# Kernel optimization log

Measured on AMD Instinct MI355X. Metric: run time of the kernel, lower is better.

Reference implementation:

```python
import jax, jax.numpy as jnp
import numpy as np

N, E, D, C, L, G = 50000, 1600000, 128, 10, 4, 512
BN_EPS = 1e-5


def setup_inputs() -> dict:
    key = jax.random.key(0)
    ks = jax.random.split(key, 16)
    s = 0.05  # weight init scale
    inp = {
        "x": jax.random.normal(ks[0], (N, D), dtype=jnp.float32),
        "edge_index": jax.random.randint(ks[1], (2, E), 0, N, dtype=jnp.int32),
        "batch": jnp.sort(jax.random.randint(ks[2], (N,), 0, G, dtype=jnp.int32)),
        "num_graphs": G,
        # GINConv inner MLP params (layer 0 input dim == D since num_features == num_hidden)
        "conv_W1": jax.random.normal(ks[3], (L, D, D), dtype=jnp.float32) * s,
        "conv_b1": jnp.zeros((L, D), dtype=jnp.float32),
        "conv_bn_g": jnp.ones((L, D), dtype=jnp.float32),
        "conv_bn_b": jnp.zeros((L, D), dtype=jnp.float32),
        "conv_W2": jax.random.normal(ks[4], (L, D, D), dtype=jnp.float32) * s,
        "conv_b2": jnp.zeros((L, D), dtype=jnp.float32),
        # outer BatchNorm after each conv
        "bn_g": jnp.ones((L, D), dtype=jnp.float32),
        "bn_b": jnp.zeros((L, D), dtype=jnp.float32),
        # per-scale classifier heads (L+1 of them; fcs[0] input dim == num_features == D)
        "fc_W": jax.random.normal(ks[5], (L + 1, D, C), dtype=jnp.float32) * s,
        "fc_b": jnp.zeros((L + 1, C), dtype=jnp.float32),
    }
    return inp


def _bn(h, g, b):
    # BatchNorm1d in training mode: batch stats over nodes, biased variance
    m = h.mean(axis=0)
    v = jnp.mean((h - m) ** 2, axis=0)
    return (h - m) * jax.lax.rsqrt(v + BN_EPS) * g + b


def reference(x, edge_index, batch, num_graphs, conv_W1, conv_b1, conv_bn_g,
              conv_bn_b, conv_W2, conv_b2, bn_g, bn_b, fc_W, fc_b):
    n_nodes = x.shape[0]
    src, dst = edge_index[0], edge_index[1]
    outs = [x]
    h = x
    for i in range(L):
        # GINConv (eps=0, aggr='add'): mlp(x + scatter_add of neighbor features)
        agg = jax.ops.segment_sum(h[src], dst, num_segments=n_nodes)  # [N, D]
        z = h + agg
        z = z @ conv_W1[i] + conv_b1[i]
        z = jax.nn.relu(_bn(z, conv_bn_g[i], conv_bn_b[i]))
        z = z @ conv_W2[i] + conv_b2[i]
        h = jax.nn.relu(_bn(z, bn_g[i], bn_b[i]))
        outs.append(h)
    out = None
    for i, o in enumerate(outs):
        pooled = jax.ops.segment_sum(o, batch, num_segments=num_graphs)  # [G, D]
        logits = pooled @ fc_W[i] + fc_b[i]
        out = logits if out is None else out + logits
    return jax.nn.log_softmax(out, axis=-1)
```

## Files before the change

kernel.cpp:

```cpp
#include <hip/hip_runtime.h>

#define NN 50000
#define EE 1600000
#define DD 128
#define CC 10
#define LLAY 4
#define GG 512
#define GD (GG*DD)
#define NB 196
#define BK_EDGES 1024
#define BUCKCAP 16000
#define NSUB 16
#define SUBW 3125
#define WPAD 136

static constexpr float BN_EPS = 1e-5f;
static constexpr float INV_N = 1.0f / (float)NN;

typedef __bf16 bf16x8 __attribute__((ext_vector_type(8)));
typedef float f32x4 __attribute__((ext_vector_type(4)));

static __device__ __forceinline__ float bflo(unsigned u){ return __uint_as_float(u << 16); }
static __device__ __forceinline__ float bfhi(unsigned u){ return __uint_as_float(u & 0xffff0000u); }
static __device__ __forceinline__ unsigned short f2bf(float f){
    unsigned u = __float_as_uint(f);
    return (unsigned short)((u + 0x7fffu + ((u >> 16) & 1u)) >> 16);
}
static __device__ __forceinline__ unsigned packbf(float a, float b){
    return (unsigned)f2bf(a) | ((unsigned)f2bf(b) << 16);
}
static __device__ __forceinline__ unsigned encf(float f){
    unsigned b = __float_as_uint(f);
    return (b & 0x80000000u) ? ~b : (b | 0x80000000u);
}
static __device__ __forceinline__ float decf(unsigned e){
    unsigned b = (e & 0x80000000u) ? (e ^ 0x80000000u) : ~e;
    return __uint_as_float(b);
}
static __device__ __forceinline__ bf16x8 ldfrag(const unsigned short* p){
    union { uint4 u; bf16x8 b; } t; t.u = *(const uint4*)p; return t.b;
}
static __device__ __forceinline__ bf16x8 asfrag(uint4 u){
    union { uint4 u; bf16x8 b; } t; t.u = u; return t.b;
}


__global__ void zero_k(int* p, int n){
    int i = blockIdx.x * 256 + threadIdx.x;
    if (i < n) p[i] = 0;
}

__global__ void wprep_k(const float* __restrict__ W1, const float* __restrict__ W2,
                        unsigned short* __restrict__ Wtall){
    int idx = blockIdx.x * 256 + threadIdx.x;
    int mat = idx >> 14; int rr = idx & 16383;
    int k = rr >> 7; int j = rr & 127;
    const float* Wsrc = (mat < 4) ? (W1 + mat * 16384) : (W2 + (mat - 4) * 16384);
    Wtall[mat * 16384 + j * 128 + k] = f2bf(Wsrc[k * 128 + j]);
}

__global__ void gsearch_k(const int* __restrict__ batch, int* __restrict__ gstart){
    int g = blockIdx.x * 256 + threadIdx.x;
    if (g <= GG){
        int lo = 0, hi = NN;
        while (lo < hi){ int mid = (lo + hi) >> 1; if (batch[mid] < g) lo = mid + 1; else hi = mid; }
        gstart[g] = lo;
    }
}

__global__ __launch_bounds__(256) void binA_k(const int* __restrict__ srcA,
                                              const int* __restrict__ dstA,
                                              int* __restrict__ bucketCur,
                                              unsigned* __restrict__ binned){
    __shared__ int cnt[NB], bas[NB], off[NB];
    int tid = threadIdx.x;
    if (tid < NB){ cnt[tid] = 0; off[tid] = 0; }
    __syncthreads();
    int e0 = blockIdx.x * BK_EDGES;
    int myDst[4], mySrc[4];
    #pragma unroll
    for (int k = 0; k < 4; k++){
        int i = tid + k * 256;
        int e = e0 + i;
        bool v = (i < BK_EDGES) && (e < EE);
        myDst[k] = v ? dstA[e] : -1;
        mySrc[k] = v ? srcA[e] : 0;
        if (myDst[k] >= 0) atomicAdd(&cnt[myDst[k] >> 8], 1);
    }
    __syncthreads();
    if (tid < NB && cnt[tid] > 0) bas[tid] = atomicAdd(&bucketCur[tid], cnt[tid]);
    __syncthreads();
    #pragma unroll
    for (int k = 0; k < 4; k++){
        int dv = myDst[k];
        if (dv >= 0){
            int b = dv >> 8;
            int p = b * BUCKCAP + bas[b] + atomicAdd(&off[b], 1);
            binned[p] = (unsigned)mySrc[k] | ((unsigned)(dv & 255) << 17);
        }
    }
}

__global__ __launch_bounds__(256) void bscan_k(const int* __restrict__ bucketCur,
                                               int* __restrict__ bucketBase,
                                               int* __restrict__ rp){
    __shared__ int lds[256];
    int t = threadIdx.x;
    int v = (t < NB) ? bucketCur[t] : 0;
    lds[t] = v; __syncthreads();
    for (int o = 1; o < 256; o <<= 1){
        int xv = 0; if (t >= o) xv = lds[t - o];
        __syncthreads(); lds[t] += xv; __syncthreads();
    }
    int excl = lds[t] - v;
    if (t < NB) bucketBase[t] = excl;
    if (t == 0){ bucketBase[NB] = EE; rp[NN] = EE; }
}

__global__ __launch_bounds__(1024) void binB_k(const unsigned* __restrict__ binned,
                                               const int* __restrict__ bucketCur,
                                               const int* __restrict__ bucketBase,
                                               int* __restrict__ rp,
                                               int* __restrict__ ssort){
    __shared__ int c16[256 * NSUB];
    __shared__ int b16[256 * NSUB];
    __shared__ int nt[256];
    int b = blockIdx.x, tid = threadIdx.x;
    int nb0 = b * 256;
    int nmax = NN - nb0; if (nmax > 256) nmax = 256;
    for (int i = tid; i < 256 * NSUB; i += 1024) c16[i] = 0;
    __syncthreads();
    int cntb = bucketCur[b];
    int src0 = b * BUCKCAP;
    int base = bucketBase[b];
    for (int i = tid; i < cntb; i += 1024){
        unsigned u = binned[src0 + i];
        int src = (int)(u & 0x1FFFFu); int dl = (int)(u >> 17);
        atomicAdd(&c16[dl * NSUB + src / SUBW], 1);
    }
    __syncthreads();
    int cc[NSUB]; int tot = 0;
    if (tid < 256){
        #pragma unroll
        for (int k = 0; k < NSUB; k++){ cc[k] = c16[tid * NSUB + k]; tot += cc[k]; }
        nt[tid] = tot;
    }
    __syncthreads();
    for (int o = 1; o < 256; o <<= 1){
        int xv = 0;
        if (tid < 256 && tid >= o) xv = nt[tid - o];
        __syncthreads();
        if (tid < 256) nt[tid] += xv;
        __syncthreads();
    }
    if (tid < 256){
        int p = base + nt[tid] - tot;
        if (tid < nmax) rp[nb0 + tid] = p;
        int run = p;
        #pragma unroll
        for (int k = 0; k < NSUB; k++){ b16[tid * NSUB + k] = run; run += cc[k]; }
    }
    __syncthreads();
    for (int i = tid; i < 256 * NSUB; i += 1024) c16[i] = 0;
    __syncthreads();
    for (int i = tid; i < cntb; i += 1024){
        unsigned u = binned[src0 + i];
        int src = (int)(u & 0x1FFFFu); int dl = (int)(u >> 17);
        int t = src / SUBW;
        int pos = b16[dl * NSUB + t] + atomicAdd(&c16[dl * NSUB + t], 1);
        ssort[pos] = src;
    }
}

__global__ __launch_bounds__(256) void xmax_k(const float* __restrict__ x,
                                              unsigned* __restrict__ xmaxE){
    __shared__ float sm[256];
    int tid = threadIdx.x;
    int col = tid & 127, rh = tid >> 7;
    float m = 0.f;
    for (int r = blockIdx.x * 2 + rh; r < NN; r += 1024)
        m = fmaxf(m, fabsf(x[r * 128 + col]));
    sm[tid] = m; __syncthreads();
    if (tid < 128){
        m = fmaxf(sm[tid], sm[tid + 128]);
        atomicMax(&xmaxE[col], __float_as_uint(m));
    }
}

__global__ void qx_k(const unsigned* __restrict__ xmaxE,
                     float* __restrict__ qD, float* __restrict__ qR){
    int c = threadIdx.x;
    float m = __uint_as_float(xmaxE[c]);
    qD[c] = m * (1.f / 127.f);
    qR[c] = (m > 0.f) ? 127.f / m : 0.f;
}

__global__ __launch_bounds__(256) void convxpool_k(const float2* __restrict__ x2,
                                                   const int* __restrict__ gstart,
                                                   unsigned short* __restrict__ h8u,
                                                   const float* __restrict__ qR0,
                                                   float* __restrict__ outp){
    __shared__ float sd[512];
    int b = blockIdx.x; int gid = b >> 2, chunk = b & 3;
    int tid = threadIdx.x; int c = tid & 63, rs = tid >> 6;
    int s = gstart[gid], e = gstart[gid + 1];
    float2 rv = ((const float2*)qR0)[c];
    float a0 = 0.f, a1 = 0.f;
    for (int n = s + chunk * 4 + rs; n < e; n += 16){
        float2 v = x2[n * 64 + c];
        int i0 = (int)rintf(v.x * rv.x) + 128; i0 = min(max(i0, 0), 255);
        int i1 = (int)rintf(v.y * rv.y) + 128; i1 = min(max(i1, 0), 255);
        h8u[n * 64 + c] = (unsigned short)(i0 | (i1 << 8));
        a0 += v.x; a1 += v.y;
    }
    sd[tid] = a0; sd[256 + tid] = a1; __syncthreads();
    if (tid < 64){
        float r0 = 0.f, r1 = 0.f;
        #pragma unroll
        for (int k2 = 0; k2 < 4; k2++){ r0 += sd[tid + 64 * k2]; r1 += sd[256 + tid + 64 * k2]; }
        atomicAdd(&outp[gid * 128 + 2 * tid], r0);
        atomicAdd(&outp[gid * 128 + 2 * tid + 1], r1);
    }
}


__global__ __launch_bounds__(256) void agg_k(const unsigned short* __restrict__ h8u,
                                             const int* __restrict__ rp,
                                             const int* __restrict__ ssort,
                                             const float* __restrict__ qD,
                                             float offv,
                                             unsigned* __restrict__ z32,
                                             float* __restrict__ zstats){
    int tid = threadIdx.x;
    if (blockIdx.x == 0) zstats[tid] = 0.f;
    int n = blockIdx.x * 4 + (tid >> 6);
    int lane = tid & 63;
    int e  = __builtin_amdgcn_readfirstlane(rp[n]);
    int e1 = __builtin_amdgcn_readfirstlane(rp[n + 1]);
    int deg = e1 - e;
    unsigned su = (unsigned)h8u[n * 64 + lane];
    unsigned acc0 = su & 0xFFu, acc1 = su >> 8;
    for (; e + 15 < e1; e += 16){
        int sA[16];
        #pragma unroll
        for (int k = 0; k < 16; k++) sA[k] = ssort[e + k];
        unsigned uA[16];
        #pragma unroll
        for (int k = 0; k < 16; k++) uA[k] = (unsigned)h8u[sA[k] * 64 + lane];
        #pragma unroll
        for (int k = 0; k < 16; k++){ acc0 += uA[k] & 0xFFu; acc1 += uA[k] >> 8; }
    }
    for (; e + 3 < e1; e += 4){
        int s0 = ssort[e], s1 = ssort[e + 1], s2 = ssort[e + 2], s3 = ssort[e + 3];
        unsigned u0 = (unsigned)h8u[s0 * 64 + lane];
        unsigned u1 = (unsigned)h8u[s1 * 64 + lane];
        unsigned u2 = (unsigned)h8u[s2 * 64 + lane];
        unsigned u3 = (unsigned)h8u[s3 * 64 + lane];
        acc0 += (u0 & 0xFFu) + (u1 & 0xFFu) + (u2 & 0xFFu) + (u3 & 0xFFu);
        acc1 += (u0 >> 8) + (u1 >> 8) + (u2 >> 8) + (u3 >> 8);
    }
    for (; e < e1; ++e){
        unsigned u0 = (unsigned)h8u[ssort[e] * 64 + lane];
        acc0 += u0 & 0xFFu; acc1 += u0 >> 8;
    }
    float2 qd = ((const float2*)qD)[lane];
    float degoff = offv * (float)(deg + 1);
    float z0 = qd.x * ((float)acc0 - degoff);
    float z1 = qd.y * ((float)acc1 - degoff);
    z32[n * 64 + lane] = packbf(z0, z1);
}

template<int TR>
__global__ __launch_bounds__(256) void gemm_k(const unsigned* __restrict__ A32,
                                              const unsigned short* __restrict__ Wtg,
                                              const float* __restrict__ bias,
                                              unsigned short* __restrict__ Cst,
                                              const float* __restrict__ stats,
                                              const float* __restrict__ gma,
                                              const float* __restrict__ bta,
                                              float* __restrict__ ostats,
                                              float* __restrict__ zstats,
                                              float* __restrict__ zpool,
                                              unsigned* __restrict__ mst){
    __shared__ __align__(16) unsigned short Wl[64 * WPAD];
    __shared__ float sred[1024];
    __shared__ __align__(16) float sl[128], tl[128];
    int tid = threadIdx.x;
    int slice = blockIdx.x & 1;
    int tileb = blockIdx.x >> 1;

    int wv = tid >> 6, lane = tid & 63;
    int rowbase = tileb * 128 + wv * 32;
    int r0 = rowbase + (lane & 15);
    int r1 = r0 + 16;
    int kd = (lane >> 4) * 4;
    uint4 va[4], vb[4];
    #pragma unroll
    for (int ks = 0; ks < 4; ks++){
        va[ks] = (r0 < NN) ? *(const uint4*)(A32 + r0 * 64 + ks * 16 + kd) : make_uint4(0,0,0,0);
        vb[ks] = (r1 < NN) ? *(const uint4*)(A32 + r1 * 64 + ks * 16 + kd) : make_uint4(0,0,0,0);
    }

    if (blockIdx.x == 0 && zstats) zstats[tid] = 0.f;
    if (zpool && blockIdx.x < 256) zpool[blockIdx.x * 256 + tid] = 0.f;
    {
        const uint4* src = (const uint4*)(Wtg + slice * 64 * 128);
        uint4* dst = (uint4*)Wl;
        #pragma unroll
        for (int i = 0; i < 4; i++){
            int idx = tid + 256 * i;
            int row = idx >> 4, c16 = idx & 15;
            dst[row * (WPAD / 8) + c16] = src[idx];
        }
    }
    if (TR && tid < 128){
        float mean = stats[tid] * INV_N;
        float q    = stats[128 + tid] * INV_N;
        float inv  = rsqrtf(q - mean * mean + BN_EPS);
        float s    = gma[tid] * inv;
        sl[tid] = s; tl[tid] = bta[tid] - mean * s;
    }
    __syncthreads();

    if (TR){
        #pragma unroll
        for (int ks = 0; ks < 4; ks++){
            int q = ks * 8 + (lane >> 4) * 2;
            float4 sA = ((const float4*)sl)[q], sB = ((const float4*)sl)[q + 1];
            float4 tA = ((const float4*)tl)[q], tB = ((const float4*)tl)[q + 1];
            float fs[8] = {sA.x, sA.y, sA.z, sA.w, sB.x, sB.y, sB.z, sB.w};
            float ft[8] = {tA.x, tA.y, tA.z, tA.w, tB.x, tB.y, tB.z, tB.w};
            unsigned* pa = (unsigned*)&va[ks];
            unsigned* pb = (unsigned*)&vb[ks];
            #pragma unroll
            for (int c = 0; c < 4; c++){
                float f0 = fmaxf(bflo(pa[c]) * fs[2*c] + ft[2*c], 0.f);
                float f1 = fmaxf(bfhi(pa[c]) * fs[2*c+1] + ft[2*c+1], 0.f);
                pa[c] = packbf(f0, f1);
                f0 = fmaxf(bflo(pb[c]) * fs[2*c] + ft[2*c], 0.f);
                f1 = fmaxf(bfhi(pb[c]) * fs[2*c+1] + ft[2*c+1], 0.f);
                pb[c] = packbf(f0, f1);
            }
        }
    }

    f32x4 acc[2][4];
    #pragma unroll
    for (int a = 0; a < 2; a++)
        #pragma unroll
        for (int b = 0; b < 4; b++) acc[a][b] = (f32x4){0.f, 0.f, 0.f, 0.f};

    #pragma unroll
    for (int ks = 0; ks < 4; ks++){
        int wk = ks * 32 + (lane >> 4) * 8;
        bf16x8 a0 = asfrag(va[ks]);
        bf16x8 a1 = asfrag(vb[ks]);
        #pragma unroll
        for (int ct = 0; ct < 4; ++ct){
            bf16x8 b = ldfrag(&Wl[(ct * 16 + (lane & 15)) * WPAD + wk]);
            acc[0][ct] = __builtin_amdgcn_mfma_f32_16x16x32_bf16(a0, b, acc[0][ct], 0, 0, 0);
            acc[1][ct] = __builtin_amdgcn_mfma_f32_16x16x32_bf16(a1, b, acc[1][ct], 0, 0, 0);
        }
    }

    int cl = lane & 15, rq = lane >> 4;
    float colS[4], colQ[4];
    #pragma unroll
    for (int ct = 0; ct < 4; ++ct){
        int col = slice * 64 + ct * 16 + cl;
        float bv = bias[col];
        float ps = 0.f, pq = 0.f;
        float vx = -3.4e38f, vn = -3.4e38f;
        #pragma unroll
        for (int rt = 0; rt < 2; ++rt){
            #pragma unroll
            for (int rr2 = 0; rr2 < 4; ++rr2){
                int grow = rowbase + rt * 16 + rq * 4 + rr2;
                if (grow < NN){
                    float val = acc[rt][ct][rr2] + bv;
                    Cst[grow * 128 + col] = f2bf(val);
                    ps += val; pq += val * val;
                    if (TR){ vx = fmaxf(vx, val); vn = fmaxf(vn, -val); }
                }
            }
        }
        ps += __shfl_xor(ps, 16); pq += __shfl_xor(pq, 16);
        ps += __shfl_xor(ps, 32); pq += __shfl_xor(pq, 32);
        colS[ct] = ps; colQ[ct] = pq;
        if (TR){
            vx = fmaxf(vx, __shfl_xor(vx, 16)); vx = fmaxf(vx, __shfl_xor(vx, 32));
            vn = fmaxf(vn, __shfl_xor(vn, 16)); vn = fmaxf(vn, __shfl_xor(vn, 32));
            if (rq == 0){
                sred[512 + wv * 64 + ct * 16 + cl] = vx;
                sred[768 + wv * 64 + ct * 16 + cl] = vn;
            }
        }
    }
    if (rq == 0){
        #pragma unroll
        for (int ct = 0; ct < 4; ++ct){
            sred[wv * 64 + ct * 16 + cl]       = colS[ct];
            sred[256 + wv * 64 + ct * 16 + cl] = colQ[ct];
        }
    }
    __syncthreads();
    if (tid < 64){
        float s1 = sred[tid] + sred[64 + tid] + sred[128 + tid] + sred[192 + tid];
        float s2 = sred[256 + tid] + sred[320 + tid] + sred[384 + tid] + sred[448 + tid];
        atomicAdd(&ostats[slice * 64 + tid], s1);
        atomicAdd(&ostats[128 + slice * 64 + tid], s2);
        if (TR){
            float mx = fmaxf(fmaxf(sred[512 + tid], sred[576 + tid]),
                             fmaxf(sred[640 + tid], sred[704 + tid]));
            float mn = fmaxf(fmaxf(sred[768 + tid], sred[832 + tid]),
                             fmaxf(sred[896 + tid], sred[960 + tid]));
            atomicMax(&mst[slice * 64 + tid], encf(mx));
            atomicMax(&mst[128 + slice * 64 + tid], encf(mn));
        }
    }
}

__global__ __launch_bounds__(256) void ewpool_k(const unsigned* __restrict__ z32,
                                                const float* __restrict__ stats,
                                                const float* __restrict__ g,
                                                const float* __restrict__ b,
                                                const int* __restrict__ gstart,
                                                unsigned short* __restrict__ h8u,
                                                const unsigned* __restrict__ mst,
                                                float* __restrict__ qDn,
                                                float* __restrict__ outp){
    __shared__ float sd[512];
    int blk = blockIdx.x; int gid = blk >> 2, chunk = blk & 3;
    int tid = threadIdx.x;
    int c = tid & 63, rs = tid >> 6;
    int c2 = c * 2;
    float m0 = stats[c2] * INV_N,     q0 = stats[128 + c2] * INV_N;
    float inv0 = rsqrtf(q0 - m0 * m0 + BN_EPS);
    float s0 = g[c2] * inv0, t0 = b[c2] - m0 * s0;
    float m1 = stats[c2 + 1] * INV_N, q1 = stats[129 + c2] * INV_N;
    float inv1 = rsqrtf(q1 - m1 * m1 + BN_EPS);
    float s1 = g[c2 + 1] * inv1, t1 = b[c2 + 1] - m1 * s1;
    float zx0 = decf(mst[c2]),      zn0 = -decf(mst[128 + c2]);
    float zx1 = decf(mst[c2 + 1]),  zn1 = -decf(mst[129 + c2]);
    float hm0 = fmaxf(fmaxf(s0 * zx0 + t0, s0 * zn0 + t0), 0.f);
    float hm1 = fmaxf(fmaxf(s1 * zx1 + t1, s1 * zn1 + t1), 0.f);
    float r80 = (hm0 > 0.f) ? 255.f / hm0 : 0.f;
    float r81 = (hm1 > 0.f) ? 255.f / hm1 : 0.f;
    if (blk == 0 && rs == 0){
        qDn[c2]     = hm0 * (1.f / 255.f);
        qDn[c2 + 1] = hm1 * (1.f / 255.f);
    }
    int s = gstart[gid], e = gstart[gid + 1];
    float a0 = 0.f, a1 = 0.f;
    int n = s + chunk * 4 + rs;
    for (; n + 16 < e; n += 32){
        unsigned u0 = z32[n * 64 + c];
        unsigned u1 = z32[(n + 16) * 64 + c];
        float f0 = fmaxf(bflo(u0) * s0 + t0, 0.f);
        float f1 = fmaxf(bfhi(u0) * s1 + t1, 0.f);
        unsigned cu0 = (unsigned)(f0 * r80 + 0.5f); if (cu0 > 255u) cu0 = 255u;
        unsigned cu1 = (unsigned)(f1 * r81 + 0.5f); if (cu1 > 255u) cu1 = 255u;
        h8u[n * 64 + c] = (unsigned short)(cu0 | (cu1 << 8));
        a0 += f0; a1 += f1;
        f0 = fmaxf(bflo(u1) * s0 + t0, 0.f);
        f1 = fmaxf(bfhi(u1) * s1 + t1, 0.f);
        cu0 = (unsigned)(f0 * r80 + 0.5f); if (cu0 > 255u) cu0 = 255u;
        cu1 = (unsigned)(f1 * r81 + 0.5f); if (cu1 > 255u) cu1 = 255u;
        h8u[(n + 16) * 64 + c] = (unsigned short)(cu0 | (cu1 << 8));
        a0 += f0; a1 += f1;
    }
    for (; n < e; n += 16){
        unsigned u = z32[n * 64 + c];
        float f0 = fmaxf(bflo(u) * s0 + t0, 0.f);
        float f1 = fmaxf(bfhi(u) * s1 + t1, 0.f);
        unsigned cu0 = (unsigned)(f0 * r80 + 0.5f); if (cu0 > 255u) cu0 = 255u;
        unsigned cu1 = (unsigned)(f1 * r81 + 0.5f); if (cu1 > 255u) cu1 = 255u;
        h8u[n * 64 + c] = (unsigned short)(cu0 | (cu1 << 8));
        a0 += f0; a1 += f1;
    }
    sd[tid] = a0; sd[256 + tid] = a1; __syncthreads();
    if (tid < 64){
        float r0 = 0.f, r1 = 0.f;
        #pragma unroll
        for (int k2 = 0; k2 < 4; k2++){ r0 += sd[tid + 64 * k2]; r1 += sd[256 + tid + 64 * k2]; }
        atomicAdd(&outp[gid * 128 + 2 * tid], r0);
        atomicAdd(&outp[gid * 128 + 2 * tid + 1], r1);
    }
}

__global__ __launch_bounds__(64) void final_k(const float* __restrict__ pooled,
                                              const float* __restrict__ fcW,
                                              const float* __restrict__ fcb,
                                              float* __restrict__ out){
    int g = blockIdx.x, l = threadIdx.x;
    float p0[5], p1[5];
    #pragma unroll
    for (int i = 0; i < 5; i++){
        p0[i] = pooled[i * GD + g * 128 + l];
        p1[i] = pooled[i * GD + g * 128 + 64 + l];
    }
    float lg[10];
    #pragma unroll
    for (int c2 = 0; c2 < 10; c2++){
        float s = 0;
        #pragma unroll
        for (int i = 0; i < 5; i++){
            s += p0[i] * fcW[(i * 128 + l) * 10 + c2];
            s += p1[i] * fcW[(i * 128 + 64 + l) * 10 + c2];
        }
        #pragma unroll
        for (int off = 32; off >= 1; off >>= 1) s += __shfl_down(s, off);
        lg[c2] = s;
    }
    if (l == 0){
        #pragma unroll
        for (int c2 = 0; c2 < 10; c2++){
            float bs = 0;
            #pragma unroll
            for (int i = 0; i < 5; i++) bs += fcb[i * 10 + c2];
            lg[c2] += bs;
        }
        float mx = lg[0];
        #pragma unroll
        for (int c2 = 1; c2 < 10; c2++) mx = fmaxf(mx, lg[c2]);
        float se = 0;
        #pragma unroll
        for (int c2 = 0; c2 < 10; c2++) se += expf(lg[c2] - mx);
        float lse = mx + logf(se);
        #pragma unroll
        for (int c2 = 0; c2 < 10; c2++) out[g * 10 + c2] = lg[c2] - lse;
    }
}


extern "C" void kernel_launch(void* const* d_in, const int* in_sizes, int n_in,
                              void* d_out, int out_size, void* d_ws, size_t ws_size,
                              hipStream_t stream){
    (void)in_sizes; (void)n_in; (void)out_size; (void)ws_size;
    const float* x     = (const float*)d_in[0];
    const int*   ei    = (const int*)d_in[1];
    const int*   batch = (const int*)d_in[2];
    const float* cW1   = (const float*)d_in[4];
    const float* cb1   = (const float*)d_in[5];
    const float* cbng  = (const float*)d_in[6];
    const float* cbnb  = (const float*)d_in[7];
    const float* cW2   = (const float*)d_in[8];
    const float* cb2   = (const float*)d_in[9];
    const float* bng   = (const float*)d_in[10];
    const float* bnb   = (const float*)d_in[11];
    const float* fcW   = (const float*)d_in[12];
    const float* fcb   = (const float*)d_in[13];

    char* base = (char*)d_ws;
    size_t off = 0;
    auto alloc = [&](size_t bytes) -> void* {
        void* p = base + off;
        off = (off + bytes + 255) & ~(size_t)255;
        return p;
    };
    unsigned*       zA     = (unsigned*)alloc((size_t)NN * 64 * 4);
    unsigned*       zB     = (unsigned*)alloc((size_t)NN * 64 * 4);
    unsigned short* h8     = (unsigned short*)alloc((size_t)NN * 64 * 2);
    unsigned short* Wtall  = (unsigned short*)alloc(8 * 16384 * 2);
    int*            ssort  = (int*)alloc((size_t)EE * 4);
    int*            rp     = (int*)alloc((NN + 1) * 4);
    int*            gstart = (int*)alloc((GG + 1) * 4);
    int*            bucketBase = (int*)alloc((NB + 1) * 4);
    int*            bucketCur  = (int*)alloc(NB * 4);
    unsigned*       xmaxE  = (unsigned*)alloc(128 * 4);
    unsigned*       mstats = (unsigned*)alloc((size_t)LLAY * 256 * 4);
    float*          pooled = (float*)alloc((size_t)5 * GD * 4);
    float*          stats1 = (float*)alloc(256 * 4);
    float*          stats2 = (float*)alloc(256 * 4);
    float*          qD     = (float*)alloc(5 * 128 * 4);
    float*          qR     = (float*)alloc(128 * 4);
    unsigned*       binned = (unsigned*)zB;

    int zwords = (int)(((char*)(pooled + GD) - (char*)bucketCur) / 4);

    zero_k<<<(zwords + 255) / 256, 256, 0, stream>>>(bucketCur, zwords);
    wprep_k<<<512, 256, 0, stream>>>(cW1, cW2, Wtall);
    gsearch_k<<<3, 256, 0, stream>>>(batch, gstart);
    binA_k<<<(EE + BK_EDGES - 1) / BK_EDGES, 256, 0, stream>>>(ei, ei + EE, bucketCur, binned);
    bscan_k<<<1, 256, 0, stream>>>(bucketCur, bucketBase, rp);
    binB_k<<<NB, 1024, 0, stream>>>(binned, bucketCur, bucketBase, rp, ssort);
    xmax_k<<<512, 256, 0, stream>>>(x, xmaxE);
    qx_k<<<1, 128, 0, stream>>>(xmaxE, qD, qR);
    convxpool_k<<<4 * GG, 256, 0, stream>>>((const float2*)x, gstart, h8, qR, pooled);

    const int gemmGrid = 2 * ((NN + 127) / 128);
    for (int i = 0; i < LLAY; i++){
        agg_k<<<NN / 4, 256, 0, stream>>>(h8, rp, ssort,
                                          qD + i * 128, (i == 0) ? 128.f : 0.f, zA, stats1);
        gemm_k<0><<<gemmGrid, 256, 0, stream>>>(zA, Wtall + i * 16384, cb1 + i * 128,
                                                (unsigned short*)zB,
                                                nullptr, nullptr, nullptr, stats1, stats2,
                                                nullptr, nullptr);
        gemm_k<1><<<gemmGrid, 256, 0, stream>>>(zB, Wtall + (4 + i) * 16384, cb2 + i * 128,
                                                (unsigned short*)zA,
                                                stats1, cbng + i * 128, cbnb + i * 128, stats2,
                                                nullptr, pooled + (size_t)(i + 1) * GD,
                                                mstats + (size_t)i * 256);
        ewpool_k<<<4 * GG, 256, 0, stream>>>(zA, stats2, bng + i * 128, bnb + i * 128,
                                             gstart, h8, mstats + (size_t)i * 256,
                                             qD + (i + 1) * 128,
                                             pooled + (size_t)(i + 1) * GD);
    }
    final_k<<<GG, 64, 0, stream>>>(pooled, fcW, fcb, (float*)d_out);
}
```

Measured before the change: 551.6 us.

## Stage binned edges in LDS for coalesced writes; halve GEMM row tile

```diff
diff --git a/kernel.cpp b/kernel.cpp
--- a/kernel.cpp
+++ b/kernel.cpp
@@ -72,32 +72,58 @@
                                               const int* __restrict__ dstA,
                                               int* __restrict__ bucketCur,
                                               unsigned* __restrict__ binned){
-    __shared__ int cnt[NB], bas[NB], off[NB];
+    __shared__ int cnt[256];
+    __shared__ int lb[256];
+    __shared__ int bas[NB];
+    __shared__ int off[NB];
+    __shared__ unsigned stage[BK_EDGES];
+    __shared__ int tots;
     int tid = threadIdx.x;
-    if (tid < NB){ cnt[tid] = 0; off[tid] = 0; }
+    cnt[tid] = 0;
+    if (tid < NB) off[tid] = 0;
     __syncthreads();
     int e0 = blockIdx.x * BK_EDGES;
-    int myDst[4], mySrc[4];
+    int myB[4]; unsigned myVal[4];
     #pragma unroll
     for (int k = 0; k < 4; k++){
-        int i = tid + k * 256;
-        int e = e0 + i;
-        bool v = (i < BK_EDGES) && (e < EE);
-        myDst[k] = v ? dstA[e] : -1;
-        mySrc[k] = v ? srcA[e] : 0;
-        if (myDst[k] >= 0) atomicAdd(&cnt[myDst[k] >> 8], 1);
-    }
-    __syncthreads();
-    if (tid < NB && cnt[tid] > 0) bas[tid] = atomicAdd(&bucketCur[tid], cnt[tid]);
+        int e = e0 + tid + k * 256;
+        bool v = (e < EE);
+        int d = v ? dstA[e] : -1;
+        int s = v ? srcA[e] : 0;
+        myB[k] = v ? (d >> 8) : -1;
+        myVal[k] = (unsigned)s | ((unsigned)(d & 255) << 17);
+        if (v) atomicAdd(&cnt[d >> 8], 1);
+    }
+    __syncthreads();
+    int v = cnt[tid];
+    lb[tid] = v; __syncthreads();
+    for (int o = 1; o < 256; o <<= 1){
+        int x = 0; if (tid >= o) x = lb[tid - o];
+        __syncthreads(); lb[tid] += x; __syncthreads();
+    }
+    int incl = lb[tid];
+    if (tid == 255) tots = incl;
+    __syncthreads();
+    lb[tid] = incl - v;
+    if (tid < NB && v > 0) bas[tid] = atomicAdd(&bucketCur[tid], v);
     __syncthreads();
     #pragma unroll
     for (int k = 0; k < 4; k++){
-        int dv = myDst[k];
-        if (dv >= 0){
-            int b = dv >> 8;
-            int p = b * BUCKCAP + bas[b] + atomicAdd(&off[b], 1);
-            binned[p] = (unsigned)mySrc[k] | ((unsigned)(dv & 255) << 17);
-        }
+        int b = myB[k];
+        if (b >= 0){
+            int p = lb[b] + atomicAdd(&off[b], 1);
+            stage[p] = myVal[k];
+        }
+    }
+    __syncthreads();
+    int tot = tots;
+    for (int i = tid; i < tot; i += 256){
+        int lo = 0, hi = NB - 1;
+        while (lo < hi){
+            int mid = (lo + hi + 1) >> 1;
+            if (lb[mid] <= i) lo = mid; else hi = mid - 1;
+        }
+        binned[lo * BUCKCAP + bas[lo] + (i - lb[lo])] = stage[i];
     }
 }
 
@@ -290,16 +316,13 @@
     int tileb = blockIdx.x >> 1;
 
     int wv = tid >> 6, lane = tid & 63;
-    int rowbase = tileb * 128 + wv * 32;
+    int rowbase = tileb * 64 + wv * 16;
     int r0 = rowbase + (lane & 15);
-    int r1 = r0 + 16;
     int kd = (lane >> 4) * 4;
-    uint4 va[4], vb[4];
-    #pragma unroll
-    for (int ks = 0; ks < 4; ks++){
+    uint4 va[4];
+    #pragma unroll
+    for (int ks = 0; ks < 4; ks++)
         va[ks] = (r0 < NN) ? *(const uint4*)(A32 + r0 * 64 + ks * 16 + kd) : make_uint4(0,0,0,0);
-        vb[ks] = (r1 < NN) ? *(const uint4*)(A32 + r1 * 64 + ks * 16 + kd) : make_uint4(0,0,0,0);
-    }
 
     if (blockIdx.x == 0 && zstats) zstats[tid] = 0.f;
     if (zpool && blockIdx.x < 256) zpool[blockIdx.x * 256 + tid] = 0.f;
@@ -331,35 +354,27 @@
             float fs[8] = {sA.x, sA.y, sA.z, sA.w, sB.x, sB.y, sB.z, sB.w};
             float ft[8] = {tA.x, tA.y, tA.z, tA.w, tB.x, tB.y, tB.z, tB.w};
             unsigned* pa = (unsigned*)&va[ks];
-            unsigned* pb = (unsigned*)&vb[ks];
             #pragma unroll
             for (int c = 0; c < 4; c++){
                 float f0 = fmaxf(bflo(pa[c]) * fs[2*c] + ft[2*c], 0.f);
                 float f1 = fmaxf(bfhi(pa[c]) * fs[2*c+1] + ft[2*c+1], 0.f);
                 pa[c] = packbf(f0, f1);
-                f0 = fmaxf(bflo(pb[c]) * fs[2*c] + ft[2*c], 0.f);
-                f1 = fmaxf(bfhi(pb[c]) * fs[2*c+1] + ft[2*c+1], 0.f);
-                pb[c] = packbf(f0, f1);
             }
         }
     }
 
-    f32x4 acc[2][4];
-    #pragma unroll
-    for (int a = 0; a < 2; a++)
-        #pragma unroll
-        for (int b = 0; b < 4; b++) acc[a][b] = (f32x4){0.f, 0.f, 0.f, 0.f};
+    f32x4 acc[4];
+    #pragma unroll
+    for (int ct = 0; ct < 4; ct++) acc[ct] = (f32x4){0.f, 0.f, 0.f, 0.f};
 
     #pragma unroll
     for (int ks = 0; ks < 4; ks++){
         int wk = ks * 32 + (lane >> 4) * 8;
         bf16x8 a0 = asfrag(va[ks]);
-        bf16x8 a1 = asfrag(vb[ks]);
         #pragma unroll
         for (int ct = 0; ct < 4; ++ct){
             bf16x8 b = ldfrag(&Wl[(ct * 16 + (lane & 15)) * WPAD + wk]);
-            acc[0][ct] = __builtin_amdgcn_mfma_f32_16x16x32_bf16(a0, b, acc[0][ct], 0, 0, 0);
-            acc[1][ct] = __builtin_amdgcn_mfma_f32_16x16x32_bf16(a1, b, acc[1][ct], 0, 0, 0);
+            acc[ct] = __builtin_amdgcn_mfma_f32_16x16x32_bf16(a0, b, acc[ct], 0, 0, 0);
         }
     }
 
@@ -372,16 +387,13 @@
         float ps = 0.f, pq = 0.f;
         float vx = -3.4e38f, vn = -3.4e38f;
         #pragma unroll
-        for (int rt = 0; rt < 2; ++rt){
-            #pragma unroll
-            for (int rr2 = 0; rr2 < 4; ++rr2){
-                int grow = rowbase + rt * 16 + rq * 4 + rr2;
-                if (grow < NN){
-                    float val = acc[rt][ct][rr2] + bv;
-                    Cst[grow * 128 + col] = f2bf(val);
-                    ps += val; pq += val * val;
-                    if (TR){ vx = fmaxf(vx, val); vn = fmaxf(vn, -val); }
-                }
+        for (int rr2 = 0; rr2 < 4; ++rr2){
+            int grow = rowbase + rq * 4 + rr2;
+            if (grow < NN){
+                float val = acc[ct][rr2] + bv;
+                Cst[grow * 128 + col] = f2bf(val);
+                ps += val; pq += val * val;
+                if (TR){ vx = fmaxf(vx, val); vn = fmaxf(vn, -val); }
             }
         }
         ps += __shfl_xor(ps, 16); pq += __shfl_xor(pq, 16);
@@ -588,7 +600,7 @@
     qx_k<<<1, 128, 0, stream>>>(xmaxE, qD, qR);
     convxpool_k<<<4 * GG, 256, 0, stream>>>((const float2*)x, gstart, h8, qR, pooled);
 
-    const int gemmGrid = 2 * ((NN + 127) / 128);
+    const int gemmGrid = 2 * ((NN + 63) / 64);
     for (int i = 0; i < LLAY; i++){
         agg_k<<<NN / 4, 256, 0, stream>>>(h8, rp, ssort,
                                           qD + i * 128, (i == 0) ? 128.f : 0.f, zA, stats1);
```

Measured after the change: 604.9 us. 9.7% more time.
